# Performance work log

Hardware: AMD Instinct MI355X
Metric: run time of the kernel (lower is better)

Reference implementation:

```python
import jax, jax.numpy as jnp
import numpy as np

N_PER_DEG = 30000
MAX_DEG = 6
MIN_DEG = 0
N_ATOMS = N_PER_DEG * (MAX_DEG + 1)  # 210000, atoms sorted by degree
N_FEAT = 128
NB_FILTER = 128
NB_AFFINE = 2 * MAX_DEG + (1 - MIN_DEG)  # 13


def setup_inputs() -> dict:
    key = jax.random.key(0)
    ks = jax.random.split(key, 2 + MAX_DEG)
    atoms = jax.random.normal(ks[0], (N_ATOMS, N_FEAT), dtype=jnp.float32)
    # glorot-ish scale for the 13 affine weights
    W = jax.random.normal(ks[1], (NB_AFFINE, N_FEAT, NB_FILTER), dtype=jnp.float32) * (1.0 / np.sqrt(N_FEAT))
    b = jnp.zeros((NB_AFFINE, NB_FILTER), dtype=jnp.float32)
    # deg_slice[d] = (start, count) for degree d in 0..MAX_DEG; equal-size buckets
    deg_slice = jnp.asarray(
        np.stack([np.arange(MAX_DEG + 1) * N_PER_DEG,
                  np.full(MAX_DEG + 1, N_PER_DEG)], axis=1).astype(np.int32))
    inp = {"atoms": atoms, "W": W, "b": b, "deg_slice": deg_slice}
    for d in range(1, MAX_DEG + 1):
        inp[f"adj{d}"] = jax.random.randint(ks[1 + d], (N_PER_DEG, d), 0, N_ATOMS, dtype=jnp.int32)
    return inp


def reference(atoms, W, b, deg_slice, adj1, adj2, adj3, adj4, adj5, adj6):
    """Degree-bucketed graph convolution (deepchem GraphConv, linear activation).

    W ordering matches the original iterator: for deg=1..MAX_DEG the pair
    (rel=W[2*(deg-1)], self=W[2*(deg-1)+1]), then deg-0 self uses W[2*MAX_DEG].
    Output concat order: deg 0 bucket first, then deg 1..MAX_DEG.
    """
    adjs = [adj1, adj2, adj3, adj4, adj5, adj6]
    ds = np.asarray(deg_slice)  # structural constant: static slice bounds
    outs = [None] * (MAX_DEG + 1 - MIN_DEG)
    # deg 0: self-affine only
    s0, c0 = int(ds[0, 0]), int(ds[0, 1])
    outs[0] = atoms[s0:s0 + c0] @ W[2 * MAX_DEG] + b[2 * MAX_DEG]
    for deg in range(1, MAX_DEG + 1):
        s, c = int(ds[deg, 0]), int(ds[deg, 1])
        # gather neighbors of each degree-deg atom and sum: (c, deg, F) -> (c, F)
        rel = jnp.take(atoms, adjs[deg - 1], axis=0).sum(axis=1)
        out = (rel @ W[2 * (deg - 1)] + b[2 * (deg - 1)]
               + atoms[s:s + c] @ W[2 * (deg - 1) + 1] + b[2 * (deg - 1) + 1])
        outs[deg] = out
    return jnp.concatenate(outs, axis=0)  # (N_ATOMS, NB_FILTER)
```

## Files before the change

### kernel.cpp

```cpp
#include <hip/hip_runtime.h>
#include <hip/hip_bf16.h>

#define NPD 30000
#define NF  128
#define MAXDEG 6
#define LDK2 264

#define WT_BLOCKS   208
#define CVT8_BLOCKS 1641

typedef __attribute__((ext_vector_type(8))) short short8;
typedef __attribute__((ext_vector_type(4))) float floatx4;

__device__ __forceinline__ unsigned short f2bf(float f) {
    __hip_bfloat16 h = __float2bfloat16(f);
    return __builtin_bit_cast(unsigned short, h);
}
__device__ __forceinline__ float bf2f(unsigned short u) {
    unsigned v = ((unsigned)u) << 16; return __builtin_bit_cast(float, v);
}
__device__ __forceinline__ uint4 pack16B(float4 a, float4 b) {
    uint4 v;
    v.x = (unsigned)f2bf(a.x) | ((unsigned)f2bf(a.y) << 16);
    v.y = (unsigned)f2bf(a.z) | ((unsigned)f2bf(a.w) << 16);
    v.z = (unsigned)f2bf(b.x) | ((unsigned)f2bf(b.y) << 16);
    v.w = (unsigned)f2bf(b.z) | ((unsigned)f2bf(b.w) << 16);
    return v;
}
__device__ __forceinline__ uint4 pack16Bv(floatx4 a, floatx4 b) {
    uint4 v;
    v.x = (unsigned)f2bf(a.x) | ((unsigned)f2bf(a.y) << 16);
    v.y = (unsigned)f2bf(a.z) | ((unsigned)f2bf(a.w) << 16);
    v.z = (unsigned)f2bf(b.x) | ((unsigned)f2bf(b.y) << 16);
    v.w = (unsigned)f2bf(b.z) | ((unsigned)f2bf(b.w) << 16);
    return v;
}
__device__ __forceinline__ void addu4(float* s, uint4 h) {
    s[0] += bf2f((unsigned short)h.x); s[1] += bf2f((unsigned short)(h.x >> 16));
    s[2] += bf2f((unsigned short)h.y); s[3] += bf2f((unsigned short)(h.y >> 16));
    s[4] += bf2f((unsigned short)h.z); s[5] += bf2f((unsigned short)(h.z >> 16));
    s[6] += bf2f((unsigned short)h.w); s[7] += bf2f((unsigned short)(h.w >> 16));
}

__device__ __forceinline__ void lgkm_barrier() {
    asm volatile("s_waitcnt lgkmcnt(0)" ::: "memory");
    __builtin_amdgcn_s_barrier();
}

__global__ __launch_bounds__(256) void prep_kernel(
    const float* __restrict__ atoms, const float* __restrict__ W,
    unsigned short* __restrict__ atomsH, unsigned short* __restrict__ Wt)
{
    __shared__ unsigned short t[32][33];
    const int bx = blockIdx.x;
    if (bx < WT_BLOCKS) {
        const int a  = bx >> 4;
        const int k0 = ((bx >> 2) & 3) * 32, n0 = (bx & 3) * 32;
        const int tx = threadIdx.x & 31, ty = threadIdx.x >> 5;
        const float*    Wp  = W  + (size_t)a * NF * NF;
        unsigned short* Wtp = Wt + (size_t)a * NF * NF;
#pragma unroll
        for (int i = 0; i < 32; i += 8)
            t[ty + i][tx] = f2bf(Wp[(size_t)(k0 + ty + i) * NF + (n0 + tx)]);
        __syncthreads();
#pragma unroll
        for (int i = 0; i < 32; i += 8)
            Wtp[(size_t)(n0 + ty + i) * NF + (k0 + tx)] = t[tx][ty + i];
    } else {
        const size_t n8   = (size_t)NPD * (MAXDEG + 1) * NF / 8;
        const size_t base = (size_t)(bx - WT_BLOCKS) * 2048 + threadIdx.x;
#pragma unroll
        for (int it = 0; it < 8; ++it) {
            const size_t i = base + (size_t)it * 256;
            if (i < n8) {
                const floatx4* p = (const floatx4*)(atoms + i * 8);
                floatx4 a = __builtin_nontemporal_load(p);
                floatx4 b = __builtin_nontemporal_load(p + 1);
                ((uint4*)atomsH)[i] = pack16Bv(a, b);
            }
        }
    }
}

template <int DEG, bool BF16A>
__device__ __forceinline__ void fused_work(
    const float* __restrict__ atomsF, const unsigned short* __restrict__ atomsH,
    const unsigned short* __restrict__ Wt, const float* __restrict__ bvec,
    const int* __restrict__ adj, float* __restrict__ out,
    unsigned short* __restrict__ sA, int bx)
{
    const int tid  = threadIdx.x;
    const int lane = tid & 63, wave = tid >> 6;
    const int nb = lane & 15;
    const int kq = (lane >> 4) * 8;
    const int col0 = wave * 32;
    const int row0 = bx * 64;
    const int v0 = min(32, NPD - row0);
    const int v1 = min(32, NPD - row0 - 32);
    const int row0g = DEG * NPD + row0;
    const int wi_self = (DEG == 0) ? 12 : (2 * DEG - 1);
    const int wi_rel  = (DEG > 0) ? 2 * (DEG - 1) : 0;

    const int r0 = tid >> 4,  ch0 = (tid & 15) * 8;
    const int r1 = r0 + 16;
    const int gr = tid >> 3,  gc = (tid & 7) * 16;

    floatx4 acc[2][2];
    auto zacc = [&]() {
#pragma unroll
        for (int i = 0; i < 2; i++)
#pragma unroll
            for (int j = 0; j < 2; j++) acc[i][j] = (floatx4){0.f, 0.f, 0.f, 0.f};
    };
    auto mma4_pre = [&](const short8 bs[4][2], int aoff) {
#pragma unroll
        for (int kk = 0; kk < 4; ++kk) {
            short8 af[2];
#pragma unroll
            for (int mt = 0; mt < 2; ++mt)
                af[mt] = *(const short8*)&sA[(mt * 16 + nb) * LDK2 + aoff + kk * 32 + kq];
#pragma unroll
            for (int mt = 0; mt < 2; ++mt)
#pragma unroll
                for (int nt = 0; nt < 2; ++nt)
                    acc[mt][nt] = __builtin_amdgcn_mfma_f32_16x16x32_bf16(
                        af[mt], bs[kk][nt], acc[mt][nt], 0, 0, 0);
        }
    };
    auto mma4_ld = [&](int wi, int aoff) {
        const unsigned short* Wp = Wt + (size_t)wi * NF * NF;
#pragma unroll
        for (int kk = 0; kk < 4; ++kk) {
            short8 bfr[2];
#pragma unroll
            for (int nt = 0; nt < 2; ++nt)
                bfr[nt] = *(const short8*)(Wp + (size_t)(col0 + nt * 16 + nb) * NF
                                              + kk * 32 + kq);
            short8 af[2];
#pragma unroll
            for (int mt = 0; mt < 2; ++mt)
                af[mt] = *(const short8*)&sA[(mt * 16 + nb) * LDK2 + aoff + kk * 32 + kq];
#pragma unroll
            for (int mt = 0; mt < 2; ++mt)
#pragma unroll
                for (int nt = 0; nt < 2; ++nt)
                    acc[mt][nt] = __builtin_amdgcn_mfma_f32_16x16x32_bf16(
                        af[mt], bfr[nt], acc[mt][nt], 0, 0, 0);
        }
    };
    float bias[2];
#pragma unroll
    for (int nt = 0; nt < 2; ++nt) {
        const int n = col0 + nt * 16 + nb;
        float bv = bvec[wi_self * NF + n];
        if (DEG > 0) bv += bvec[wi_rel * NF + n];
        bias[nt] = bv;
    }
    const int rq = (lane >> 4) * 4;
    auto epilogue = [&](int vlim, int toff) {
#pragma unroll
        for (int mt = 0; mt < 2; ++mt) {
#pragma unroll
            for (int reg = 0; reg < 4; ++reg) {
                const int r = mt * 16 + rq + reg;
                if (r < vlim) {
                    float* op = out + (size_t)(row0g + toff + r) * NF;
#pragma unroll
                    for (int nt = 0; nt < 2; ++nt)
                        __builtin_nontemporal_store(acc[mt][nt][reg] + bias[nt],
                                                    op + col0 + nt * 16 + nb);
                }
            }
        }
    };

    if constexpr (BF16A) {
        uint4 s0a = *(const uint4*)(atomsH + (size_t)(row0g + min(r0, v0 - 1)) * NF + ch0);
        uint4 s0b = *(const uint4*)(atomsH + (size_t)(row0g + min(r1, v0 - 1)) * NF + ch0);

        int idx0[DEG > 0 ? DEG : 1];
        if constexpr (DEG > 0) {
            const int* arow = adj + (size_t)(row0 + min(gr, v0 - 1)) * DEG;
#pragma unroll
            for (int j = 0; j < DEG; ++j) idx0[j] = arow[j];
        }
        short8 bs[4][2];
        {
            const unsigned short* Wp = Wt + (size_t)wi_self * NF * NF;
#pragma unroll
            for (int kk = 0; kk < 4; ++kk)
#pragma unroll
                for (int nt = 0; nt < 2; ++nt)
                    bs[kk][nt] = *(const short8*)(Wp + (size_t)(col0 + nt * 16 + nb) * NF
                                                     + kk * 32 + kq);
        }

        if constexpr (DEG > 0) {
            uint4 ga[DEG], gb[DEG];
#pragma unroll
            for (int j = 0; j < DEG; ++j) {
                const unsigned short* base = atomsH + (size_t)idx0[j] * NF + gc;
                ga[j] = *(const uint4*)base;
                gb[j] = *(const uint4*)(base + 8);
            }
            *(uint4*)&sA[r0 * LDK2 + ch0] = s0a;
            *(uint4*)&sA[r1 * LDK2 + ch0] = s0b;
            lgkm_barrier();
            zacc();
            mma4_pre(bs, 0);

            float s[16];
#pragma unroll
            for (int i = 0; i < 16; ++i) s[i] = 0.f;
#pragma unroll
            for (int j = 0; j < DEG; ++j) { addu4(s, ga[j]); addu4(s + 8, gb[j]); }
            *(uint4*)&sA[gr * LDK2 + NF + gc]     = pack16B(
                make_float4(s[0], s[1], s[2], s[3]), make_float4(s[4], s[5], s[6], s[7]));
            *(uint4*)&sA[gr * LDK2 + NF + gc + 8] = pack16B(
                make_float4(s[8], s[9], s[10], s[11]), make_float4(s[12], s[13], s[14], s[15]));

            uint4 s1a, s1b;
            int idx1[DEG];
            if (v1 > 0) {
                s1a = *(const uint4*)(atomsH + (size_t)(row0g + 32 + min(r0, v1 - 1)) * NF + ch0);
                s1b = *(const uint4*)(atomsH + (size_t)(row0g + 32 + min(r1, v1 - 1)) * NF + ch0);
                const int* arow1 = adj + (size_t)(row0 + 32 + min(gr, v1 - 1)) * DEG;
#pragma unroll
                for (int j = 0; j < DEG; ++j) idx1[j] = arow1[j];
            }
            lgkm_barrier();
            mma4_ld(wi_rel, NF);
            epilogue(v0, 0);

            if (v1 > 0) {
                uint4 ga1[DEG], gb1[DEG];
#pragma unroll
                for (int j = 0; j < DEG; ++j) {
                    const unsigned short* base = atomsH + (size_t)idx1[j] * NF + gc;
                    ga1[j] = *(const uint4*)base;
                    gb1[j] = *(const uint4*)(base + 8);
                }
                lgkm_barrier();
                *(uint4*)&sA[r0 * LDK2 + ch0] = s1a;
                *(uint4*)&sA[r1 * LDK2 + ch0] = s1b;
                lgkm_barrier();
                zacc();
                mma4_pre(bs, 0);

                float s2[16];
#pragma unroll
                for (int i = 0; i < 16; ++i) s2[i] = 0.f;
#pragma unroll
                for (int j = 0; j < DEG; ++j) { addu4(s2, ga1[j]); addu4(s2 + 8, gb1[j]); }
                *(uint4*)&sA[gr * LDK2 + NF + gc]     = pack16B(
                    make_float4(s2[0], s2[1], s2[2], s2[3]),
                    make_float4(s2[4], s2[5], s2[6], s2[7]));
                *(uint4*)&sA[gr * LDK2 + NF + gc + 8] = pack16B(
                    make_float4(s2[8], s2[9], s2[10], s2[11]),
                    make_float4(s2[12], s2[13], s2[14], s2[15]));
                lgkm_barrier();
                mma4_ld(wi_rel, NF);
                epilogue(v1, 32);
            }
        } else {
            uint4 s1a, s1b;
            if (v1 > 0) {
                s1a = *(const uint4*)(atomsH + (size_t)(row0g + 32 + min(r0, v1 - 1)) * NF + ch0);
                s1b = *(const uint4*)(atomsH + (size_t)(row0g + 32 + min(r1, v1 - 1)) * NF + ch0);
            }
            *(uint4*)&sA[r0 * LDK2 + ch0] = s0a;
            *(uint4*)&sA[r1 * LDK2 + ch0] = s0b;
            lgkm_barrier();
            zacc();
            mma4_pre(bs, 0);
            epilogue(v0, 0);
            if (v1 > 0) {
                lgkm_barrier();
                *(uint4*)&sA[r0 * LDK2 + ch0] = s1a;
                *(uint4*)&sA[r1 * LDK2 + ch0] = s1b;
                lgkm_barrier();
                zacc();
                mma4_pre(bs, 0);
                epilogue(v1, 32);
            }
        }
    } else {
        for (int t = 0; t < 2; ++t) {
            const int vt = (t == 0) ? v0 : v1;
            if (vt <= 0) break;
            const int toff = t * 32;
            if (t) __syncthreads();
            const float4* sp0 = (const float4*)(atomsF + (size_t)(row0g + toff + min(r0, vt - 1)) * NF + ch0);
            const float4* sp1 = (const float4*)(atomsF + (size_t)(row0g + toff + min(r1, vt - 1)) * NF + ch0);
            float4 a0 = sp0[0], a1 = sp0[1], a2 = sp1[0], a3 = sp1[1];
            *(uint4*)&sA[r0 * LDK2 + ch0] = pack16B(a0, a1);
            *(uint4*)&sA[r1 * LDK2 + ch0] = pack16B(a2, a3);
            if constexpr (DEG > 0) {
                const int* arow = adj + (size_t)(row0 + toff + min(gr, vt - 1)) * DEG;
                int idxs[DEG];
#pragma unroll
                for (int j = 0; j < DEG; ++j) idxs[j] = arow[j];
                float s[16];
#pragma unroll
                for (int i = 0; i < 16; ++i) s[i] = 0.f;
#pragma unroll
                for (int j = 0; j < DEG; ++j) {
                    const float4* p = (const float4*)(atomsF + (size_t)idxs[j] * NF + gc);
                    float4 q0 = p[0], q1 = p[1], q2 = p[2], q3 = p[3];
                    s[0]  += q0.x; s[1]  += q0.y; s[2]  += q0.z; s[3]  += q0.w;
                    s[4]  += q1.x; s[5]  += q1.y; s[6]  += q1.z; s[7]  += q1.w;
                    s[8]  += q2.x; s[9]  += q2.y; s[10] += q2.z; s[11] += q2.w;
                    s[12] += q3.x; s[13] += q3.y; s[14] += q3.z; s[15] += q3.w;
                }
                *(uint4*)&sA[gr * LDK2 + NF + gc]     = pack16B(
                    make_float4(s[0], s[1], s[2], s[3]), make_float4(s[4], s[5], s[6], s[7]));
                *(uint4*)&sA[gr * LDK2 + NF + gc + 8] = pack16B(
                    make_float4(s[8], s[9], s[10], s[11]), make_float4(s[12], s[13], s[14], s[15]));
            }
            __syncthreads();
            zacc();
            mma4_ld(wi_self, 0);
            if constexpr (DEG > 0) mma4_ld(wi_rel, NF);
            epilogue(vt, toff);
        }
    }
}

template <bool BF16A>
__global__ __launch_bounds__(256) void fused_kernel(
    const float* __restrict__ atomsF, const unsigned short* __restrict__ atomsH,
    const unsigned short* __restrict__ Wt, const float* __restrict__ bvec,
    const int* __restrict__ adj1, const int* __restrict__ adj2,
    const int* __restrict__ adj3, const int* __restrict__ adj4,
    const int* __restrict__ adj5, const int* __restrict__ adj6,
    float* __restrict__ out)
{
    __shared__ unsigned short sA[32 * LDK2];
    const int bid = blockIdx.x;
    const int deg = bid % 7, bx = bid / 7;
    switch (deg) {
        case 0: fused_work<0, BF16A>(atomsF, atomsH, Wt, bvec, nullptr, out, sA, bx); break;
        case 1: fused_work<1, BF16A>(atomsF, atomsH, Wt, bvec, adj1,    out, sA, bx); break;
        case 2: fused_work<2, BF16A>(atomsF, atomsH, Wt, bvec, adj2,    out, sA, bx); break;
        case 3: fused_work<3, BF16A>(atomsF, atomsH, Wt, bvec, adj3,    out, sA, bx); break;
        case 4: fused_work<4, BF16A>(atomsF, atomsH, Wt, bvec, adj4,    out, sA, bx); break;
        case 5: fused_work<5, BF16A>(atomsF, atomsH, Wt, bvec, adj5,    out, sA, bx); break;
        default: fused_work<6, BF16A>(atomsF, atomsH, Wt, bvec, adj6,   out, sA, bx); break;
    }
}

__global__ __launch_bounds__(128) void naive_kernel(
    const float* __restrict__ atoms, const float* __restrict__ W,
    const float* __restrict__ b,
    const int* __restrict__ adj1, const int* __restrict__ adj2,
    const int* __restrict__ adj3, const int* __restrict__ adj4,
    const int* __restrict__ adj5, const int* __restrict__ adj6,
    float* __restrict__ out)
{
    const int i = blockIdx.x;
    const int deg = i / NPD, r = i - deg * NPD, n = threadIdx.x;
    __shared__ float selfr[NF], relr[NF];
    selfr[n] = atoms[(size_t)i * NF + n];
    float rv = 0.f;
    if (deg > 0) {
        const int* adjs[6] = {adj1, adj2, adj3, adj4, adj5, adj6};
        const int* adj = adjs[deg - 1];
        for (int j = 0; j < deg; ++j)
            rv += atoms[(size_t)adj[(size_t)r * deg + j] * NF + n];
    }
    relr[n] = rv;
    __syncthreads();
    const int ws  = (deg == 0) ? 12 : 2 * deg - 1;
    const int wrl = 2 * (deg - 1);
    float acc = b[ws * NF + n] + ((deg > 0) ? b[wrl * NF + n] : 0.f);
    for (int k = 0; k < NF; ++k) {
        acc += selfr[k] * W[(size_t)ws * NF * NF + (size_t)k * NF + n];
        if (deg > 0) acc += relr[k] * W[(size_t)wrl * NF * NF + (size_t)k * NF + n];
    }
    out[(size_t)i * NF + n] = acc;
}

extern "C" void kernel_launch(void* const* d_in, const int* in_sizes, int n_in,
                              void* d_out, int out_size, void* d_ws, size_t ws_size,
                              hipStream_t stream) {
    const float* atoms = (const float*)d_in[0];
    const float* W     = (const float*)d_in[1];
    const float* b     = (const float*)d_in[2];
    const int* adj1 = (const int*)d_in[4];
    const int* adj2 = (const int*)d_in[5];
    const int* adj3 = (const int*)d_in[6];
    const int* adj4 = (const int*)d_in[7];
    const int* adj5 = (const int*)d_in[8];
    const int* adj6 = (const int*)d_in[9];

    const size_t wt_bytes = (size_t)13 * NF * NF * sizeof(unsigned short);
    const size_t at_bytes = (size_t)NPD * (MAXDEG + 1) * NF * sizeof(unsigned short);
    const int gxB = (NPD + 63) / 64;

    if (ws_size >= wt_bytes + at_bytes) {
        unsigned short* Wt     = (unsigned short*)d_ws;
        unsigned short* atomsH = (unsigned short*)((char*)d_ws + wt_bytes);
        prep_kernel<<<WT_BLOCKS + CVT8_BLOCKS, 256, 0, stream>>>(atoms, W, atomsH, Wt);
        fused_kernel<true><<<gxB * 7, 256, 0, stream>>>(
            atoms, atomsH, Wt, b, adj1, adj2, adj3, adj4, adj5, adj6, (float*)d_out);
    } else if (ws_size >= wt_bytes) {
        unsigned short* Wt = (unsigned short*)d_ws;
        prep_kernel<<<WT_BLOCKS, 256, 0, stream>>>(atoms, W, nullptr, Wt);
        fused_kernel<false><<<gxB * 7, 256, 0, stream>>>(
            atoms, nullptr, Wt, b, adj1, adj2, adj3, adj4, adj5, adj6, (float*)d_out);
    } else {
        naive_kernel<<<NPD * (MAXDEG + 1), NF, 0, stream>>>(
            atoms, W, b, adj1, adj2, adj3, adj4, adj5, adj6, (float*)d_out);
    }
}
```

Before: 258.9 us.

## Process four 32-row tiles per block with double-buffered LDS pipelining

Each block now handles four 32-row tiles instead of two, and alternates between two LDS buffers so the next tile's self rows and neighbor gathers are loaded while the current tile runs its MFMA work. The self-weight B fragments stay in registers and are reused across more tiles, and one barrier per tile is removed. The cost is a doubled LDS footprint, higher register pressure from the prefetched data, and fewer blocks, which reduces parallelism across the GPU.

```diff
diff --git a/kernel.cpp b/kernel.cpp
--- a/kernel.cpp
+++ b/kernel.cpp
@@ -5,6 +5,8 @@
 #define NF  128
 #define MAXDEG 6
 #define LDK2 264
+#define TLDS (32 * LDK2)
+#define NT   4
 
 #define WT_BLOCKS   208
 #define CVT8_BLOCKS 1641
@@ -94,13 +96,15 @@
     const int nb = lane & 15;
     const int kq = (lane >> 4) * 8;
     const int col0 = wave * 32;
-    const int row0 = bx * 64;
-    const int v0 = min(32, NPD - row0);
-    const int v1 = min(32, NPD - row0 - 32);
+    const int row0 = bx * (32 * NT);
     const int row0g = DEG * NPD + row0;
     const int wi_self = (DEG == 0) ? 12 : (2 * DEG - 1);
     const int wi_rel  = (DEG > 0) ? 2 * (DEG - 1) : 0;
 
+    int v[NT];
+#pragma unroll
+    for (int t = 0; t < NT; ++t) v[t] = min(32, NPD - row0 - 32 * t);
+
     const int r0 = tid >> 4,  ch0 = (tid & 15) * 8;
     const int r1 = r0 + 16;
     const int gr = tid >> 3,  gc = (tid & 7) * 16;
@@ -112,13 +116,13 @@
 #pragma unroll
             for (int j = 0; j < 2; j++) acc[i][j] = (floatx4){0.f, 0.f, 0.f, 0.f};
     };
-    auto mma4_pre = [&](const short8 bs[4][2], int aoff) {
+    auto mma4_pre = [&](const short8 bs[4][2], const unsigned short* buf, int aoff) {
 #pragma unroll
         for (int kk = 0; kk < 4; ++kk) {
             short8 af[2];
 #pragma unroll
             for (int mt = 0; mt < 2; ++mt)
-                af[mt] = *(const short8*)&sA[(mt * 16 + nb) * LDK2 + aoff + kk * 32 + kq];
+                af[mt] = *(const short8*)&buf[(mt * 16 + nb) * LDK2 + aoff + kk * 32 + kq];
 #pragma unroll
             for (int mt = 0; mt < 2; ++mt)
 #pragma unroll
@@ -127,7 +131,7 @@
                         af[mt], bs[kk][nt], acc[mt][nt], 0, 0, 0);
         }
     };
-    auto mma4_ld = [&](int wi, int aoff) {
+    auto mma4_ld = [&](int wi, const unsigned short* buf, int aoff) {
         const unsigned short* Wp = Wt + (size_t)wi * NF * NF;
 #pragma unroll
         for (int kk = 0; kk < 4; ++kk) {
@@ -139,7 +143,7 @@
             short8 af[2];
 #pragma unroll
             for (int mt = 0; mt < 2; ++mt)
-                af[mt] = *(const short8*)&sA[(mt * 16 + nb) * LDK2 + aoff + kk * 32 + kq];
+                af[mt] = *(const short8*)&buf[(mt * 16 + nb) * LDK2 + aoff + kk * 32 + kq];
 #pragma unroll
             for (int mt = 0; mt < 2; ++mt)
 #pragma unroll
@@ -175,15 +179,9 @@
     };
 
     if constexpr (BF16A) {
-        uint4 s0a = *(const uint4*)(atomsH + (size_t)(row0g + min(r0, v0 - 1)) * NF + ch0);
-        uint4 s0b = *(const uint4*)(atomsH + (size_t)(row0g + min(r1, v0 - 1)) * NF + ch0);
-
-        int idx0[DEG > 0 ? DEG : 1];
-        if constexpr (DEG > 0) {
-            const int* arow = adj + (size_t)(row0 + min(gr, v0 - 1)) * DEG;
-#pragma unroll
-            for (int j = 0; j < DEG; ++j) idx0[j] = arow[j];
-        }
+        uint4 sa = *(const uint4*)(atomsH + (size_t)(row0g + min(r0, v[0] - 1)) * NF + ch0);
+        uint4 sb = *(const uint4*)(atomsH + (size_t)(row0g + min(r1, v[0] - 1)) * NF + ch0);
+
         short8 bs[4][2];
         {
             const unsigned short* Wp = Wt + (size_t)wi_self * NF * NF;
@@ -196,97 +194,115 @@
         }
 
         if constexpr (DEG > 0) {
+            int idxN[DEG];
             uint4 ga[DEG], gb[DEG];
-#pragma unroll
-            for (int j = 0; j < DEG; ++j) {
-                const unsigned short* base = atomsH + (size_t)idx0[j] * NF + gc;
-                ga[j] = *(const uint4*)base;
-                gb[j] = *(const uint4*)(base + 8);
-            }
-            *(uint4*)&sA[r0 * LDK2 + ch0] = s0a;
-            *(uint4*)&sA[r1 * LDK2 + ch0] = s0b;
+            {
+                const int* arow = adj + (size_t)(row0 + min(gr, v[0] - 1)) * DEG;
+                int idxC[DEG];
+#pragma unroll
+                for (int j = 0; j < DEG; ++j) idxC[j] = arow[j];
+#pragma unroll
+                for (int j = 0; j < DEG; ++j) {
+                    const unsigned short* base = atomsH + (size_t)idxC[j] * NF + gc;
+                    ga[j] = *(const uint4*)base;
+                    gb[j] = *(const uint4*)(base + 8);
+                }
+            }
+            *(uint4*)&sA[r0 * LDK2 + ch0] = sa;
+            *(uint4*)&sA[r1 * LDK2 + ch0] = sb;
+            uint4 na, nb2;
+            if (v[1] > 0) {
+                na  = *(const uint4*)(atomsH + (size_t)(row0g + 32 + min(r0, v[1] - 1)) * NF + ch0);
+                nb2 = *(const uint4*)(atomsH + (size_t)(row0g + 32 + min(r1, v[1] - 1)) * NF + ch0);
+                const int* arow = adj + (size_t)(row0 + 32 + min(gr, v[1] - 1)) * DEG;
+#pragma unroll
+                for (int j = 0; j < DEG; ++j) idxN[j] = arow[j];
+            }
             lgkm_barrier();
-            zacc();
-            mma4_pre(bs, 0);
-
-            float s[16];
-#pragma unroll
-            for (int i = 0; i < 16; ++i) s[i] = 0.f;
-#pragma unroll
-            for (int j = 0; j < DEG; ++j) { addu4(s, ga[j]); addu4(s + 8, gb[j]); }
-            *(uint4*)&sA[gr * LDK2 + NF + gc]     = pack16B(
-                make_float4(s[0], s[1], s[2], s[3]), make_float4(s[4], s[5], s[6], s[7]));
-            *(uint4*)&sA[gr * LDK2 + NF + gc + 8] = pack16B(
-                make_float4(s[8], s[9], s[10], s[11]), make_float4(s[12], s[13], s[14], s[15]));
-
-            uint4 s1a, s1b;
-            int idx1[DEG];
-            if (v1 > 0) {
-                s1a = *(const uint4*)(atomsH + (size_t)(row0g + 32 + min(r0, v1 - 1)) * NF + ch0);
-                s1b = *(const uint4*)(atomsH + (size_t)(row0g + 32 + min(r1, v1 - 1)) * NF + ch0);
-                const int* arow1 = adj + (size_t)(row0 + 32 + min(gr, v1 - 1)) * DEG;
-#pragma unroll
-                for (int j = 0; j < DEG; ++j) idx1[j] = arow1[j];
+
+#pragma unroll
+            for (int t = 0; t < NT; ++t) {
+                if (v[t] <= 0) break;
+                unsigned short* buf = sA + (t & 1) * TLDS;
+                zacc();
+                mma4_pre(bs, buf, 0);
+
+                float s[16];
+#pragma unroll
+                for (int i = 0; i < 16; ++i) s[i] = 0.f;
+#pragma unroll
+                for (int j = 0; j < DEG; ++j) { addu4(s, ga[j]); addu4(s + 8, gb[j]); }
+                *(uint4*)&buf[gr * LDK2 + NF + gc]     = pack16B(
+                    make_float4(s[0], s[1], s[2], s[3]),
+                    make_float4(s[4], s[5], s[6], s[7]));
+                *(uint4*)&buf[gr * LDK2 + NF + gc + 8] = pack16B(
+                    make_float4(s[8], s[9], s[10], s[11]),
+                    make_float4(s[12], s[13], s[14], s[15]));
+
+                const bool hasN = (t + 1 < NT) && (v[t + 1] > 0);
+                if (hasN) {
+#pragma unroll
+                    for (int j = 0; j < DEG; ++j) {
+                        const unsigned short* base = atomsH + (size_t)idxN[j] * NF + gc;
+                        ga[j] = *(const uint4*)base;
+                        gb[j] = *(const uint4*)(base + 8);
+                    }
+                }
+                lgkm_barrier();
+                mma4_ld(wi_rel, buf, NF);
+                epilogue(v[t], 32 * t);
+
+                if (hasN) {
+                    unsigned short* nbuf = sA + ((t + 1) & 1) * TLDS;
+                    *(uint4*)&nbuf[r0 * LDK2 + ch0] = na;
+                    *(uint4*)&nbuf[r1 * LDK2 + ch0] = nb2;
+                    if (t + 2 < NT && v[t + 2] > 0) {
+                        na  = *(const uint4*)(atomsH + (size_t)(row0g + 32 * (t + 2)
+                                              + min(r0, v[t + 2] - 1)) * NF + ch0);
+                        nb2 = *(const uint4*)(atomsH + (size_t)(row0g + 32 * (t + 2)
+                                              + min(r1, v[t + 2] - 1)) * NF + ch0);
+                        const int* arow = adj + (size_t)(row0 + 32 * (t + 2)
+                                              + min(gr, v[t + 2] - 1)) * DEG;
+#pragma unroll
+                        for (int j = 0; j < DEG; ++j) idxN[j] = arow[j];
+                    }
+                    lgkm_barrier();
+                }
+            }
+        } else {
+            *(uint4*)&sA[r0 * LDK2 + ch0] = sa;
+            *(uint4*)&sA[r1 * LDK2 + ch0] = sb;
+            uint4 na, nb2;
+            if (v[1] > 0) {
+                na  = *(const uint4*)(atomsH + (size_t)(row0g + 32 + min(r0, v[1] - 1)) * NF + ch0);
+                nb2 = *(const uint4*)(atomsH + (size_t)(row0g + 32 + min(r1, v[1] - 1)) * NF + ch0);
             }
             lgkm_barrier();
-            mma4_ld(wi_rel, NF);
-            epilogue(v0, 0);
-
-            if (v1 > 0) {
-                uint4 ga1[DEG], gb1[DEG];
-#pragma unroll
-                for (int j = 0; j < DEG; ++j) {
-                    const unsigned short* base = atomsH + (size_t)idx1[j] * NF + gc;
-                    ga1[j] = *(const uint4*)base;
-                    gb1[j] = *(const uint4*)(base + 8);
-                }
-                lgkm_barrier();
-                *(uint4*)&sA[r0 * LDK2 + ch0] = s1a;
-                *(uint4*)&sA[r1 * LDK2 + ch0] = s1b;
-                lgkm_barrier();
+#pragma unroll
+            for (int t = 0; t < NT; ++t) {
+                if (v[t] <= 0) break;
+                unsigned short* buf = sA + (t & 1) * TLDS;
                 zacc();
-                mma4_pre(bs, 0);
-
-                float s2[16];
-#pragma unroll
-                for (int i = 0; i < 16; ++i) s2[i] = 0.f;
-#pragma unroll
-                for (int j = 0; j < DEG; ++j) { addu4(s2, ga1[j]); addu4(s2 + 8, gb1[j]); }
-                *(uint4*)&sA[gr * LDK2 + NF + gc]     = pack16B(
-                    make_float4(s2[0], s2[1], s2[2], s2[3]),
-                    make_float4(s2[4], s2[5], s2[6], s2[7]));
-                *(uint4*)&sA[gr * LDK2 + NF + gc + 8] = pack16B(
-                    make_float4(s2[8], s2[9], s2[10], s2[11]),
-                    make_float4(s2[12], s2[13], s2[14], s2[15]));
-                lgkm_barrier();
-                mma4_ld(wi_rel, NF);
-                epilogue(v1, 32);
-            }
-        } else {
-            uint4 s1a, s1b;
-            if (v1 > 0) {
-                s1a = *(const uint4*)(atomsH + (size_t)(row0g + 32 + min(r0, v1 - 1)) * NF + ch0);
-                s1b = *(const uint4*)(atomsH + (size_t)(row0g + 32 + min(r1, v1 - 1)) * NF + ch0);
-            }
-            *(uint4*)&sA[r0 * LDK2 + ch0] = s0a;
-            *(uint4*)&sA[r1 * LDK2 + ch0] = s0b;
-            lgkm_barrier();
-            zacc();
-            mma4_pre(bs, 0);
-            epilogue(v0, 0);
-            if (v1 > 0) {
-                lgkm_barrier();
-                *(uint4*)&sA[r0 * LDK2 + ch0] = s1a;
-                *(uint4*)&sA[r1 * LDK2 + ch0] = s1b;
-                lgkm_barrier();
-                zacc();
-                mma4_pre(bs, 0);
-                epilogue(v1, 32);
+                mma4_pre(bs, buf, 0);
+                epilogue(v[t], 32 * t);
+                const bool hasN = (t + 1 < NT) && (v[t + 1] > 0);
+                if (hasN) {
+                    unsigned short* nbuf = sA + ((t + 1) & 1) * TLDS;
+                    *(uint4*)&nbuf[r0 * LDK2 + ch0] = na;
+                    *(uint4*)&nbuf[r1 * LDK2 + ch0] = nb2;
+                    if (t + 2 < NT && v[t + 2] > 0) {
+                        na  = *(const uint4*)(atomsH + (size_t)(row0g + 32 * (t + 2)
+                                              + min(r0, v[t + 2] - 1)) * NF + ch0);
+                        nb2 = *(const uint4*)(atomsH + (size_t)(row0g + 32 * (t + 2)
+                                              + min(r1, v[t + 2] - 1)) * NF + ch0);
+                    }
+                    lgkm_barrier();
+                }
             }
         }
     } else {
-        for (int t = 0; t < 2; ++t) {
-            const int vt = (t == 0) ? v0 : v1;
+        for (int t = 0; t < NT; ++t) {
+            const int vt = v[t];
             if (vt <= 0) break;
             const int toff = t * 32;
             if (t) __syncthreads();
@@ -319,8 +335,8 @@
             }
             __syncthreads();
             zacc();
-            mma4_ld(wi_self, 0);
-            if constexpr (DEG > 0) mma4_ld(wi_rel, NF);
+            mma4_ld(wi_self, sA, 0);
+            if constexpr (DEG > 0) mma4_ld(wi_rel, sA, NF);
             epilogue(vt, toff);
         }
     }
@@ -335,7 +351,7 @@
     const int* __restrict__ adj5, const int* __restrict__ adj6,
     float* __restrict__ out)
 {
-    __shared__ unsigned short sA[32 * LDK2];
+    __shared__ unsigned short sA[2 * TLDS];
     const int bid = blockIdx.x;
     const int deg = bid % 7, bx = bid / 7;
     switch (deg) {
@@ -395,7 +411,7 @@
 
     const size_t wt_bytes = (size_t)13 * NF * NF * sizeof(unsigned short);
     const size_t at_bytes = (size_t)NPD * (MAXDEG + 1) * NF * sizeof(unsigned short);
-    const int gxB = (NPD + 63) / 64;
+    const int gxB = (NPD + 32 * NT - 1) / (32 * NT);
 
     if (ws_size >= wt_bytes + at_bytes) {
         unsigned short* Wt     = (unsigned short*)d_ws;
```

Measured after the change: 267.3 us. +3.3%, slower.
